# Kernel optimization log

Measured on AMD Instinct MI355X. Metric: run time of the kernel, lower is better.

The kernel has to match this reference:

```python
import jax, jax.numpy as jnp
import numpy as np

L = 2
S = (L + 1) ** 2            # 9 spherical harmonic coefficients
C = 128                     # sphere_channels
H = 128                     # hidden_channels
NH = 8                      # num_heads
A = 32                      # attn_alpha_channels
V = 16                      # attn_value_channels
N = 5000                    # nodes
E = 50000                   # edges
DE = 128                    # invariant edge embedding dim
G = 18                      # S2 grid points

# l of each coefficient in l-major layout [S]
L_OF = np.concatenate([np.full(2 * l + 1, l) for l in range(L + 1)])
IDX_M0 = np.array([l * l + l for l in range(L + 1)])

def _idx_m(m):
    neg = np.array([l * l + l - m for l in range(m, L + 1)])
    pos = np.array([l * l + l + m for l in range(m, L + 1)])
    return neg, pos

IDX_M1_NEG, IDX_M1_POS = _idx_m(1)
IDX_M2_NEG, IDX_M2_POS = _idx_m(2)
# m-major ordering and its inverse permutation back to l-major
PERM = np.concatenate([IDX_M0, IDX_M1_POS, IDX_M1_NEG, IDX_M2_POS, IDX_M2_NEG])
INV_PERM = np.argsort(PERM)


def _silu(x):
    return x * jax.nn.sigmoid(x)


def _layernorm(x, g, b, eps=1e-5):
    mu = x.mean(-1, keepdims=True)
    var = ((x - mu) ** 2).mean(-1, keepdims=True)
    return (x - mu) * jax.lax.rsqrt(var + eps) * g + b


def _smooth_leaky_relu(x, a=0.2):
    return 0.5 * (1 + a) * x + 0.5 * (1 - a) * x * (2 * jax.nn.sigmoid(x) - 1)


def _so2_conv(x, w_m0, b_m0, w_m1, w_m2, cout):
    """SO(2) convolution on rotated embeddings. x: [E,S,Cin] l-major.
    Returns ([E,S,cout] l-major, extra m=0 channels)."""
    e = x.shape[0]
    # m = 0: plain linear over flattened (L+1)*Cin
    x0 = x[:, IDX_M0, :].reshape(e, -1)
    y0 = x0 @ w_m0 + b_m0
    y0_main = y0[:, : (L + 1) * cout].reshape(e, L + 1, cout)
    y0_extra = y0[:, (L + 1) * cout:]
    parts = [y0_main]
    # m > 0: complex (cos/sin) SO2 mixing with shared weight for real/imag
    for neg, pos, w in ((IDX_M1_NEG, IDX_M1_POS, w_m1), (IDX_M2_NEG, IDX_M2_POS, w_m2)):
        nl = len(neg)
        xr = x[:, pos, :].reshape(e, -1)
        xi = x[:, neg, :].reshape(e, -1)
        yr = xr @ w  # [E, 2*nl*cout]
        yi = xi @ w
        yr_r, yr_i = yr[:, : nl * cout], yr[:, nl * cout:]
        yi_r, yi_i = yi[:, : nl * cout], yi[:, nl * cout:]
        parts.append((yr_r - yi_i).reshape(e, nl, cout))   # +m (real)
        parts.append((yr_i + yi_r).reshape(e, nl, cout))   # -m (imag)
    out_m = jnp.concatenate(parts, axis=1)                 # m-major
    return out_m[:, INV_PERM, :], y0_extra


def _s2_act(x, togrid, fromgrid):
    g = jnp.einsum('gs,esc->egc', togrid, x)
    return jnp.einsum('sg,egc->esc', fromgrid, _silu(g))


def _sep_s2_act(scalars, x, togrid, fromgrid):
    t = _s2_act(x, togrid, fromgrid)
    return jnp.concatenate([_silu(scalars)[:, None, :], t[:, 1:, :]], axis=1)


def _so3_linear(x, w, b):
    # w: [L+1, Cin, Cout], shared across m within each l; bias only on l=0
    out = jnp.einsum('nsc,sco->nso', x, w[L_OF])
    return out.at[:, 0, :].add(b)


def _eqv_norm(x, g, b, eps=1e-5):
    # l=0: layernorm over channels; l>0: RMS over (m, channels) per degree
    outs = [_layernorm(x[:, 0:1, :], g[0], b)]
    for l in range(1, L + 1):
        sl = x[:, l * l:(l + 1) * (l + 1), :]
        rms = jnp.sqrt(jnp.mean(sl ** 2, axis=(1, 2), keepdims=True) + eps)
        outs.append(sl / rms * g[l])
    return jnp.concatenate(outs, axis=1)


def _forward(x, edge_distance, wigner, rad_w1, rad_b1, rad_ln_g, rad_ln_b, rad_w2, rad_b2,
             w1_m0, b1_m0, w1_m1, w1_m2, w2_m0, b2_m0, w2_m1, w2_m2,
             alpha_ln_g, alpha_ln_b, alpha_dot, proj_w, proj_b,
             norm1_g, norm1_b, norm2_g, norm2_b,
             gate_w, gate_b, ffn_w1, ffn_b1, ffn_w2, ffn_b2,
             togrid, fromgrid, edge_src, edge_dst):
    # ---------- SO2 equivariant graph attention ----------
    xn = _eqv_norm(x, norm1_g, norm1_b)
    msg = jnp.concatenate([xn[edge_src], xn[edge_dst]], axis=-1)      # [E,S,2C]
    msg = jnp.einsum('eij,ejc->eic', wigner, msg)                     # rotate to edge frame
    # radial function shared across m within each l (use_m_share_rad)
    h = _silu(_layernorm(edge_distance @ rad_w1 + rad_b1, rad_ln_g, rad_ln_b))
    rad = (h @ rad_w2 + rad_b2).reshape(-1, L + 1, 2 * C)             # [E,L+1,2C]
    msg = msg * rad[:, L_OF, :]
    hid, x0_extra = _so2_conv(msg, w1_m0, b1_m0, w1_m1, w1_m2, H)
    x_alpha = x0_extra[:, : NH * A].reshape(-1, NH, A)
    gating = x0_extra[:, NH * A:]                                     # [E,H]
    hid = _sep_s2_act(gating, hid, togrid, fromgrid)
    val, _ = _so2_conv(hid, w2_m0, b2_m0, w2_m1, w2_m2, NH * V)
    val = jnp.einsum('eji,ejc->eic', wigner, val)                     # rotate back (D^T)
    # attention weights with per-destination segment softmax
    a = _smooth_leaky_relu(_layernorm(x_alpha, alpha_ln_g, alpha_ln_b))
    a = jnp.einsum('eha,ha->eh', a, alpha_dot)                        # [E,NH]
    amax = jax.ops.segment_max(a, edge_dst, num_segments=N)
    aexp = jnp.exp(a - amax[edge_dst])
    asum = jax.ops.segment_sum(aexp, edge_dst, num_segments=N)
    attn = aexp / asum[edge_dst]
    msg_out = (val.reshape(-1, S, NH, V) * attn[:, None, :, None]).reshape(-1, S, NH * V)
    node = jax.ops.segment_sum(msg_out, edge_dst, num_segments=N)     # [N,S,NH*V]
    x = x + _so3_linear(node, proj_w, proj_b)
    # ---------- spherical FFN (sep S2 gating) ----------
    xn = _eqv_norm(x, norm2_g, norm2_b)
    gating = xn[:, 0, :] @ gate_w + gate_b
    hh = _so3_linear(xn, ffn_w1, ffn_b1)
    hh = _sep_s2_act(gating, hh, togrid, fromgrid)
    return x + _so3_linear(hh, ffn_w2, ffn_b2)


def setup_inputs() -> dict:
    key = jax.random.key(0)
    ks = iter(jax.random.split(key, 64))
    def nrm(shape, scale=1.0):
        return jax.random.normal(next(ks), shape, dtype=jnp.float32) * scale
    EX = NH * A + H
    inp = {}
    inp['x'] = nrm((N, S, C))
    inp['edge_distance'] = nrm((E, DE))
    inp['wigner'] = nrm((E, S, S), 1.0 / np.sqrt(S))
    inp['rad_w1'] = nrm((DE, 64), 1.0 / np.sqrt(DE)); inp['rad_b1'] = jnp.zeros((64,), jnp.float32)
    inp['rad_ln_g'] = jnp.ones((64,), jnp.float32); inp['rad_ln_b'] = jnp.zeros((64,), jnp.float32)
    inp['rad_w2'] = nrm((64, 2 * C * (L + 1)), 0.05); inp['rad_b2'] = jnp.ones((2 * C * (L + 1),), jnp.float32)
    inp['w1_m0'] = nrm(((L + 1) * 2 * C, (L + 1) * H + EX), 1.0 / np.sqrt((L + 1) * 2 * C))
    inp['b1_m0'] = jnp.zeros(((L + 1) * H + EX,), jnp.float32)
    inp['w1_m1'] = nrm((2 * 2 * C, 2 * 2 * H), 1.0 / np.sqrt(2 * 2 * C))
    inp['w1_m2'] = nrm((2 * C, 2 * H), 1.0 / np.sqrt(2 * C))
    inp['w2_m0'] = nrm(((L + 1) * H, (L + 1) * NH * V), 1.0 / np.sqrt((L + 1) * H))
    inp['b2_m0'] = jnp.zeros(((L + 1) * NH * V,), jnp.float32)
    inp['w2_m1'] = nrm((2 * H, 2 * 2 * NH * V), 1.0 / np.sqrt(2 * H))
    inp['w2_m2'] = nrm((H, 2 * NH * V), 1.0 / np.sqrt(H))
    inp['alpha_ln_g'] = jnp.ones((A,), jnp.float32); inp['alpha_ln_b'] = jnp.zeros((A,), jnp.float32)
    inp['alpha_dot'] = nrm((NH, A), 1.0 / np.sqrt(A))
    inp['proj_w'] = nrm((L + 1, NH * V, C), 1.0 / np.sqrt(NH * V)); inp['proj_b'] = jnp.zeros((C,), jnp.float32)
    inp['norm1_g'] = jnp.ones((L + 1, C), jnp.float32); inp['norm1_b'] = jnp.zeros((C,), jnp.float32)
    inp['norm2_g'] = jnp.ones((L + 1, C), jnp.float32); inp['norm2_b'] = jnp.zeros((C,), jnp.float32)
    inp['gate_w'] = nrm((C, H), 1.0 / np.sqrt(C)); inp['gate_b'] = jnp.zeros((H,), jnp.float32)
    inp['ffn_w1'] = nrm((L + 1, C, H), 1.0 / np.sqrt(C)); inp['ffn_b1'] = jnp.zeros((H,), jnp.float32)
    inp['ffn_w2'] = nrm((L + 1, H, C), 1.0 / np.sqrt(H)); inp['ffn_b2'] = jnp.zeros((C,), jnp.float32)
    inp['togrid'] = nrm((G, S), 1.0 / np.sqrt(S))
    inp['fromgrid'] = nrm((S, G), 1.0 / np.sqrt(G))
    inp['edge_src'] = jax.random.randint(next(ks), (E,), 0, N)
    inp['edge_dst'] = jax.random.randint(next(ks), (E,), 0, N)
    return inp


def reference(x, edge_distance, wigner, rad_w1, rad_b1, rad_ln_g, rad_ln_b, rad_w2, rad_b2,
              w1_m0, b1_m0, w1_m1, w1_m2, w2_m0, b2_m0, w2_m1, w2_m2,
              alpha_ln_g, alpha_ln_b, alpha_dot, proj_w, proj_b,
              norm1_g, norm1_b, norm2_g, norm2_b,
              gate_w, gate_b, ffn_w1, ffn_b1, ffn_w2, ffn_b2,
              togrid, fromgrid, edge_src, edge_dst):
    return _forward(x, edge_distance, wigner, rad_w1, rad_b1, rad_ln_g, rad_ln_b, rad_w2, rad_b2,
                    w1_m0, b1_m0, w1_m1, w1_m2, w2_m0, b2_m0, w2_m1, w2_m2,
                    alpha_ln_g, alpha_ln_b, alpha_dot, proj_w, proj_b,
                    norm1_g, norm1_b, norm2_g, norm2_b,
                    gate_w, gate_b, ffn_w1, ffn_b1, ffn_w2, ffn_b2,
                    togrid, fromgrid, edge_src, edge_dst)
```

## Files before the change

kernel.cpp:

```cpp
#include <hip/hip_runtime.h>
#include <hip/hip_bf16.h>

typedef unsigned short u16;
typedef unsigned int   u32;
typedef __attribute__((ext_vector_type(8))) short short8;
typedef __attribute__((ext_vector_type(4))) float float4v;

#define NN 5000
#define EE 50000

__device__ __forceinline__ float b2f(u16 u){ return __uint_as_float(((u32)u)<<16); }
__device__ __forceinline__ u16 f2b(float f){
  u32 x = __float_as_uint(f);
  u32 r = (x + 0x7fffu + ((x>>16)&1u)) >> 16;
  return (u16)r;
}
__device__ __forceinline__ float ldin(const void* p, size_t i, bool f32){
  return f32 ? ((const float*)p)[i] : b2f(((const u16*)p)[i]);
}
__device__ __forceinline__ float siluf(float x){ return x/(1.f+__expf(-x)); }
__device__ __forceinline__ float waveRedSum(float v){
  #pragma unroll
  for (int m=32;m>=1;m>>=1) v += __shfl_xor(v,m,64);
  return v;
}
__device__ __forceinline__ float red32(float v){
  #pragma unroll
  for (int m=16;m>=1;m>>=1) v += __shfl_xor(v,m,64);
  return v;
}
__device__ __forceinline__ void gload_lds16(const u16* g, u16* l){
  __builtin_amdgcn_global_load_lds((const __attribute__((address_space(1))) void*)g,
                                   (__attribute__((address_space(3))) void*)l, 16, 0, 0);
}


__global__ __launch_bounds__(256) void zero_kernel(float* __restrict__ p, int n){
  for (int i = blockIdx.x*256 + threadIdx.x; i < n; i += gridDim.x*256) p[i] = 0.f;
}

__global__ void detect_kernel(const u32* __restrict__ ng, int* __restrict__ flag){
  if (blockIdx.x == 0 && threadIdx.x == 0) *flag = (ng[0] == 0x3F800000u) ? 1 : 0;
}

__global__ __launch_bounds__(256) void hist_kernel(const int* __restrict__ edst,
    int* __restrict__ counts){
  int e = blockIdx.x*256 + threadIdx.x;
  if (e < EE) atomicAdd(&counts[edst[e]], 1);
}

__global__ __launch_bounds__(1024) void scan_kernel(const int* __restrict__ counts,
    int* __restrict__ row_start, int* __restrict__ cursor){
  __shared__ int buf[1024];
  __shared__ int base;
  const int t = threadIdx.x;
  if (t == 0){ base = 0; row_start[0] = 0; }
  __syncthreads();
  for (int i0 = 0; i0 < NN; i0 += 1024){
    int i = i0 + t;
    int c = (i < NN) ? counts[i] : 0;
    buf[t] = c;
    __syncthreads();
    #pragma unroll
    for (int ofs = 1; ofs < 1024; ofs <<= 1){
      int v = (t >= ofs) ? buf[t-ofs] : 0;
      __syncthreads();
      buf[t] += v;
      __syncthreads();
    }
    if (i < NN){
      int incl = base + buf[t];
      row_start[i+1] = incl;
      cursor[i] = incl - c;
    }
    __syncthreads();
    if (t == 0) base += buf[1023];
    __syncthreads();
  }
}

__global__ __launch_bounds__(256) void place_kernel(const int* __restrict__ edst,
    int* __restrict__ cursor, int* __restrict__ order){
  int e = blockIdx.x*256 + threadIdx.x;
  if (e < EE) order[atomicAdd(&cursor[edst[e]], 1)] = e;
}

__global__ __launch_bounds__(256) void gathercvt_kernel(const int* __restrict__ dflag,
    const void* __restrict__ src, const int* __restrict__ order, int e0,
    u16* __restrict__ dst, int n){
  const bool f32 = (*dflag != 0);
  for (int i = blockIdx.x*256 + threadIdx.x; i < n; i += gridDim.x*256){
    int le = i >> 7, c = i & 127;
    int eg = order[e0 + le];
    dst[i] = f2b(ldin(src, (size_t)eg*128 + c, f32));
  }
}

__device__ __forceinline__ void do_cvtT(bool f32, const void* src, u16* dst,
    int K, int N, int tid, int stride){
  int total = K*N;
  for (int i = tid; i < total; i += stride){
    int n = i / K, k = i - n*K;
    dst[i] = f2b(ldin(src, (size_t)k*N + n, f32));
  }
}
__device__ __forceinline__ void do_cvtT3(bool f32, const void* src, u16* dst,
    int tid, int stride){
  for (int i = tid; i < 49152; i += stride){
    int l = i >> 14, j = i & 16383;
    int n = j >> 7, k = j & 127;
    dst[i] = f2b(ldin(src, (size_t)l*16384 + (size_t)k*128 + n, f32));
  }
}
__device__ __forceinline__ void do_wprepT(bool f32, const void* w, u16* wt,
    int K0, int N0, int tid, int stride){
  int total = 4*N0*K0;
  for (int i = tid; i < total; i += stride){
    int c = i / (2*K0), rr0 = i - c*2*K0;
    float v;
    if (rr0 < K0) v = ldin(w, (size_t)rr0*2*N0 + c, f32);
    else {
      int rr = rr0 - K0;
      if (c < N0) v = -ldin(w, (size_t)rr*2*N0 + N0 + c, f32);
      else        v =  ldin(w, (size_t)rr*2*N0 + (c - N0), f32);
    }
    wt[i] = f2b(v);
  }
}

__global__ __launch_bounds__(256) void prep_all_kernel(const int* __restrict__ dflag,
    const void* w1_m0, const void* w2_m0, const void* rad_w1, const void* rad_w2,
    const void* proj_w, const void* ffn_w1, const void* ffn_w2, const void* gate_w,
    const void* b1, const void* b2, const void* rb1, const void* rb2,
    const void* pb, const void* gb, const void* f1, const void* f2,
    const void* w1_m1, const void* w1_m2, const void* w2_m1, const void* w2_m2,
    u16* w1m0T, u16* w2m0T, u16* rw1T, u16* rw2T,
    u16* projT3, u16* ffn1T3, u16* ffn2T3, u16* gateT,
    u16* b1m0C, u16* b2m0C, u16* rb1C, u16* rb2C,
    u16* pbC, u16* gbC, u16* fb1C, u16* fb2C,
    u16* W1cT, u16* W2cT, u16* W3cT, u16* W4cT){
  const bool f32 = (*dflag != 0);
  const int tid = blockIdx.x*256 + threadIdx.x;
  const int stride = gridDim.x*256;
  switch (blockIdx.y){
    case 0:  do_cvtT (f32, w1_m0, w1m0T, 768, 768, tid, stride); break;
    case 1:  do_cvtT (f32, w2_m0, w2m0T, 384, 384, tid, stride); break;
    case 2:  do_cvtT (f32, rad_w1, rw1T, 128, 64,  tid, stride); break;
    case 3:  do_cvtT (f32, rad_w2, rw2T, 64, 768,  tid, stride); break;
    case 4:  do_cvtT3(f32, proj_w, projT3, tid, stride); break;
    case 5:  do_cvtT3(f32, ffn_w1, ffn1T3, tid, stride); break;
    case 6:  do_cvtT3(f32, ffn_w2, ffn2T3, tid, stride); break;
    case 7:  do_cvtT (f32, gate_w, gateT, 128, 128, tid, stride); break;
    case 8:
      if (tid < 768) b1m0C[tid] = f2b(ldin(b1, tid, f32));
      if (tid < 384) b2m0C[tid] = f2b(ldin(b2, tid, f32));
      if (tid < 64)  rb1C[tid]  = f2b(ldin(rb1, tid, f32));
      if (tid < 768) rb2C[tid]  = f2b(ldin(rb2, tid, f32));
      if (tid < 128){
        pbC[tid]  = f2b(ldin(pb, tid, f32));
        gbC[tid]  = f2b(ldin(gb, tid, f32));
        fb1C[tid] = f2b(ldin(f1, tid, f32));
        fb2C[tid] = f2b(ldin(f2, tid, f32));
      }
      break;
    case 9:  do_wprepT(f32, w1_m1, W1cT, 512, 256, tid, stride); break;
    case 10: do_wprepT(f32, w1_m2, W2cT, 256, 128, tid, stride); break;
    case 11: do_wprepT(f32, w2_m1, W3cT, 256, 256, tid, stride); break;
    case 12: do_wprepT(f32, w2_m2, W4cT, 128, 128, tid, stride); break;
  }
}

__global__ __launch_bounds__(128) void eqvnorm_kernel(const int* __restrict__ dflag,
    const void* __restrict__ x, int in_always_f32,
    const void* __restrict__ g, const void* __restrict__ b,
    void* __restrict__ out, int out_f32){
  const bool f32 = (*dflag != 0);
  const bool inf32 = in_always_f32 || f32;
  const int n = blockIdx.x, t = threadIdx.x;
  __shared__ float red[2];
  float v[9];
  #pragma unroll
  for (int s=0;s<9;s++) v[s] = ldin(x, (size_t)n*1152 + s*128 + t, inf32);

  auto bsum = [&](float val)->float{
    float w = waveRedSum(val);
    __syncthreads();
    if ((t & 63) == 0) red[t>>6] = w;
    __syncthreads();
    return red[0] + red[1];
  };
  auto store = [&](int idx, float val){
    if (out_f32) ((float*)out)[(size_t)n*1152 + idx] = val;
    else         ((u16*) out)[(size_t)n*1152 + idx] = f2b(val);
  };
  float mu  = bsum(v[0]) * (1.f/128.f);
  float d0  = v[0] - mu;
  float var = bsum(d0*d0) * (1.f/128.f);
  store(t, d0 * rsqrtf(var + 1e-5f) * ldin(g, t, f32) + ldin(b, t, f32));
  float ss1 = v[1]*v[1] + v[2]*v[2] + v[3]*v[3];
  float inv1 = rsqrtf(bsum(ss1)*(1.f/384.f) + 1e-5f);
  float g1 = ldin(g, 128 + t, f32);
  #pragma unroll
  for (int s=1;s<=3;s++) store(s*128 + t, v[s]*inv1*g1);
  float ss2 = 0.f;
  #pragma unroll
  for (int s=4;s<9;s++) ss2 += v[s]*v[s];
  float inv2 = rsqrtf(bsum(ss2)*(1.f/640.f) + 1e-5f);
  float g2 = ldin(g, 256 + t, f32);
  #pragma unroll
  for (int s=4;s<9;s++) store(s*128 + t, v[s]*inv2*g2);
}

__global__ __launch_bounds__(256) void gemm_mfma_kernel(
    const u16* __restrict__ A, int lda, int K,
    const u16* __restrict__ Wt, int NOUT,
    const u16* __restrict__ bias,
    u16* __restrict__ out0, int ld0, int coloff0, int split,
    u16* __restrict__ out1, int ld1, int M){
  __shared__ __align__(16) u16 As[2][128*32];
  __shared__ __align__(16) u16 Bs[2][128*32];
  const int t = threadIdx.x;
  const int nxg = gridDim.x, nyg = gridDim.y;
  const int nwg = nxg * nyg;
  const int bid = blockIdx.y * nxg + blockIdx.x;
  const int q = nwg >> 3, r = nwg & 7;
  const int xcd = bid & 7, sid = bid >> 3;
  const int swz = (xcd < r ? xcd*(q+1) : r*(q+1) + (xcd - r)*q) + sid;
  const int mt = swz / nyg;
  const int r0 = mt * 128;
  const int n0 = (swz - mt*nyg) * 128;
  const int lane = t & 63, wave = t >> 6;
  const int wr = (wave & 1) * 64, wn = (wave >> 1) * 64;
  float4v acc[4][4];
  #pragma unroll
  for (int i=0;i<4;i++)
    #pragma unroll
    for (int j=0;j<4;j++) acc[i][j] = (float4v){0.f,0.f,0.f,0.f};

  const int fr = lane & 15, fq = (lane >> 4) * 8;

  const int Rw   = wave * 32;
  const int srow = lane >> 2;
  const int scol = (lane & 3) * 8;
  const u16* aG0 = A  + (size_t)(r0 + Rw + srow) * lda + scol;
  const u16* aG1 = aG0 + (size_t)16 * lda;
  const bool aV0 = (r0 + Rw + srow)      < M;
  const bool aV1 = (r0 + Rw + 16 + srow) < M;
  const u16* bG0 = Wt + (size_t)(n0 + Rw + srow) * K + scol;
  const u16* bG1 = bG0 + (size_t)16 * K;
  const bool bV0 = (n0 + Rw + srow)      < NOUT;
  const bool bV1 = (n0 + Rw + 16 + srow) < NOUT;

  auto stage = [&](int buf, int k0){
    u16* lA = &As[buf][Rw * 32];
    u16* lB = &Bs[buf][Rw * 32];
    if (aV0) gload_lds16(aG0 + k0, lA);
    if (aV1) gload_lds16(aG1 + k0, lA + 16*32);
    if (bV0) gload_lds16(bG0 + k0, lB);
    if (bV1) gload_lds16(bG1 + k0, lB + 16*32);
  };

  stage(0, 0);
  __syncthreads();
  int cur = 0;
  for (int k0 = 0; k0 < K; k0 += 32){
    const int k1 = k0 + 32;
    if (k1 < K) stage(cur ^ 1, k1);
    short8 af[4], bfv[4];
    #pragma unroll
    for (int i=0;i<4;i++){
      af[i]  = *(const short8*)&As[cur][(wr + i*16 + fr)*32 + fq];
      bfv[i] = *(const short8*)&Bs[cur][(wn + i*16 + fr)*32 + fq];
    }
    #pragma unroll
    for (int i=0;i<4;i++)
      #pragma unroll
      for (int j=0;j<4;j++)
        acc[i][j] = __builtin_amdgcn_mfma_f32_16x16x32_bf16(af[i], bfv[j], acc[i][j], 0, 0, 0);
    __syncthreads();
    cur ^= 1;
  }
  const int quad = lane >> 4;
  #pragma unroll
  for (int j=0;j<4;j++){
    int col = n0 + wn + j*16 + fr;
    if (col >= NOUT) continue;
    float bv = bias ? b2f(bias[col]) : 0.f;
    #pragma unroll
    for (int i=0;i<4;i++){
      int rbase = r0 + wr + i*16 + quad*4;
      #pragma unroll
      for (int rg=0; rg<4; rg++){
        int row = rbase + rg;
        if (row >= M) continue;
        float v = acc[i][j][rg] + bv;
        if (col < split) out0[(size_t)row*ld0 + coloff0 + col] = f2b(v);
        else             out1[(size_t)row*ld1 + (col - split)] = f2b(v);
      }
    }
  }
}

__global__ __launch_bounds__(256) void gemm_node_kernel(
    const int* __restrict__ dflag,
    const u16* __restrict__ A,
    const u16* __restrict__ W3t,
    const u16* __restrict__ bias,
    const void* __restrict__ resid, int resid_mode,
    void* __restrict__ out, int out_mode, int gate_out){
  const bool f32 = (*dflag != 0);
  const int l = blockIdx.y;
  const int rpn  = (l==0) ? 1 : ((l==1) ? 3 : 5);
  const int soff = (l==0) ? 0 : ((l==1) ? 1 : 4);
  const int M = NN * rpn;
  const int r0 = blockIdx.x * 128;
  if (r0 >= M) return;
  __shared__ __align__(16) u16 As[128][40];
  __shared__ __align__(16) u16 Bs[128][40];
  const int t = threadIdx.x;
  const int lane = t & 63, wave = t >> 6;
  const int wr = (wave & 1) * 64, wn = (wave >> 1) * 64;
  float4v acc[4][4];
  #pragma unroll
  for (int i=0;i<4;i++)
    #pragma unroll
    for (int j=0;j<4;j++) acc[i][j] = (float4v){0.f,0.f,0.f,0.f};

  const int sr = t >> 2, sc = (t & 3) * 8;
  const int fr = lane & 15, fq = (lane >> 4) * 8;
  size_t abase[2]; bool aval[2];
  #pragma unroll
  for (int s2=0;s2<2;s2++){
    int m = r0 + sr + s2*64;
    aval[s2] = m < M;
    int n = m / rpn, srow = soff + (m % rpn);
    abase[s2] = (size_t)n*1152 + srow*128 + sc;
  }
  const u16* Wl = W3t + (size_t)l*16384;

  #pragma unroll
  for (int k0 = 0; k0 < 128; k0 += 32){
    #pragma unroll
    for (int s2=0;s2<2;s2++){
      int row = sr + s2*64;
      uint4 av = make_uint4(0u,0u,0u,0u);
      if (aval[s2]) av = *(const uint4*)(A + abase[s2] + k0);
      *(uint4*)&As[row][sc] = av;
      uint4 wv = *(const uint4*)(Wl + (size_t)row*128 + k0 + sc);
      *(uint4*)&Bs[row][sc] = wv;
    }
    __syncthreads();
    short8 af[4], bfr[4];
    #pragma unroll
    for (int i=0;i<4;i++){
      af[i]  = *(const short8*)&As[wr + i*16 + fr][fq];
      bfr[i] = *(const short8*)&Bs[wn + i*16 + fr][fq];
    }
    #pragma unroll
    for (int i=0;i<4;i++)
      #pragma unroll
      for (int j=0;j<4;j++)
        acc[i][j] = __builtin_amdgcn_mfma_f32_16x16x32_bf16(af[i], bfr[j], acc[i][j], 0, 0, 0);
    __syncthreads();
  }
  const int quad = lane >> 4;
  #pragma unroll
  for (int j=0;j<4;j++){
    int col = wn + j*16 + fr;
    float bv = (bias && l==0) ? b2f(bias[col]) : 0.f;
    #pragma unroll
    for (int i=0;i<4;i++){
      int rbase = r0 + wr + i*16 + quad*4;
      #pragma unroll
      for (int rg=0; rg<4; rg++){
        int m = rbase + rg;
        if (m >= M) continue;
        int n = m / rpn, srow = soff + (m % rpn);
        size_t na = (size_t)n*1152 + srow*128 + col;
        float v = acc[i][j][rg] + bv;
        if (resid_mode == 1)      v += ((const float*)resid)[na];
        else if (resid_mode == 2) v += ldin(resid, na, f32);
        if (gate_out)            ((u16*)out)[(size_t)n*128 + col] = f2b(v);
        else if (out_mode == 0)  ((u16*)out)[na] = f2b(v);
        else if (out_mode == 1)  ((float*)out)[na] = v;
        else { if (f32) ((float*)out)[na] = v; else ((u16*)out)[na] = f2b(v); }
      }
    }
  }
}

__global__ __launch_bounds__(256) void nodecvt_kernel(const float* __restrict__ node,
    const float* __restrict__ nsum, u16* __restrict__ nodeb){
  for (int i = blockIdx.x*256 + threadIdx.x; i < NN*1152; i += gridDim.x*256){
    int n = i / 1152, c = i & 127, h = c >> 4;
    float ns = nsum[(size_t)n*8 + h];
    float rs = (ns > 0.f) ? 1.f/ns : 0.f;
    nodeb[i] = f2b(node[i] * rs);
  }
}

__global__ __launch_bounds__(128) void node_s2act_kernel(const int* __restrict__ dflag,
    const u16* __restrict__ hh, const u16* __restrict__ gating,
    const void* __restrict__ tg, const void* __restrict__ fg, u16* __restrict__ hh2){
  const bool f32 = (*dflag != 0);
  const int n = blockIdx.x, t = threadIdx.x;
  __shared__ float TG[162], FG[162];
  for (int i=t; i<162; i+=128){ TG[i]=ldin(tg,i,f32); FG[i]=ldin(fg,i,f32); }
  float hv[9];
  #pragma unroll
  for (int s=0;s<9;s++) hv[s] = b2f(hh[(size_t)n*1152 + s*128 + t]);
  __syncthreads();
  float gg[18];
  #pragma unroll
  for (int gi=0;gi<18;gi++){
    float a = 0.f;
    #pragma unroll
    for (int s=0;s<9;s++) a = fmaf(TG[gi*9+s], hv[s], a);
    gg[gi] = siluf(a);
  }
  hh2[(size_t)n*1152 + t] = f2b(siluf(b2f(gating[(size_t)n*128 + t])));
  #pragma unroll
  for (int s=1;s<9;s++){
    float a = 0.f;
    #pragma unroll
    for (int gi=0;gi<18;gi++) a = fmaf(FG[s*18+gi], gg[gi], a);
    hh2[(size_t)n*1152 + s*128 + t] = f2b(a);
  }
}

__global__ __launch_bounds__(256) void lnsilu_kernel(const int* __restrict__ dflag,
    u16* __restrict__ H, const void* __restrict__ rlng, const void* __restrict__ rlnb, int M){
  const bool f32 = (*dflag != 0);
  const int r = blockIdx.x*4 + (threadIdx.x >> 6), lane = threadIdx.x & 63;
  if (r >= M) return;
  float h = b2f(H[(size_t)r*64 + lane]);
  float mu = waveRedSum(h) * (1.f/64.f);
  float d = h - mu;
  float var = waveRedSum(d*d) * (1.f/64.f);
  float hn = d * rsqrtf(var + 1e-5f) * ldin(rlng, lane, f32) + ldin(rlnb, lane, f32);
  H[(size_t)r*64 + lane] = f2b(siluf(hn));
}

__global__ __launch_bounds__(256) void edge_rot_kernel(const int* __restrict__ dflag,
    const u16* __restrict__ xn, const void* __restrict__ wig,
    const u16* __restrict__ rad,
    const int* __restrict__ esrc, const int* __restrict__ edst,
    const int* __restrict__ order, int e0, u16* __restrict__ msg){
  const bool f32 = (*dflag != 0);
  const int le = blockIdx.x, t = threadIdx.x;
  const int eg = order[e0 + le];
  __shared__ float W[81];
  if (t < 81) W[t] = ldin(wig, (size_t)eg*81 + t, f32);
  const int src = esrc[eg], dst = edst[eg];
  float pre[9];
  const u16* base = (t < 128) ? (xn + (size_t)src*1152 + t) : (xn + (size_t)dst*1152 + (t-128));
  #pragma unroll
  for (int j=0;j<9;j++) pre[j] = b2f(base[j*128]);
  __syncthreads();
  float rot[9];
  #pragma unroll
  for (int i=0;i<9;i++){
    float a = 0.f;
    #pragma unroll
    for (int j=0;j<9;j++) a = fmaf(W[i*9+j], pre[j], a);
    rot[i] = a;
  }
  float r[3];
  #pragma unroll
  for (int l=0;l<3;l++) r[l] = b2f(rad[(size_t)le*768 + l*256 + t]);
  const int INVP[9] = {0,5,1,3,8,6,2,4,7};
  const int LOF[9]  = {0,1,1,1,2,2,2,2,2};
  u16* mb = msg + (size_t)le*2304 + t;
  #pragma unroll
  for (int i=0;i<9;i++) mb[INVP[i]*256] = f2b(rot[i] * r[LOF[i]]);
}

__global__ __launch_bounds__(256) void s2act_alpha_kernel(const int* __restrict__ dflag,
    const u16* __restrict__ hid, const u16* __restrict__ extra,
    const void* __restrict__ togrid, const void* __restrict__ fromgrid,
    const void* __restrict__ alng, const void* __restrict__ alnb, const void* __restrict__ adot,
    const int* __restrict__ edst, const int* __restrict__ order, int e0,
    u16* __restrict__ hid2, float* __restrict__ aexp, float* __restrict__ nsum){
  const bool f32 = (*dflag != 0);
  const int le = blockIdx.x, t = threadIdx.x;
  const int p = e0 + le;
  __shared__ float TG[162], FG[162];
  if (t < 162){ TG[t] = ldin(togrid, t, f32); FG[t] = ldin(fromgrid, t, f32); }
  {
    const int h = t >> 5, ai = t & 31;
    float v = b2f(extra[(size_t)le*384 + t]);
    float mu = red32(v) * (1.f/32.f);
    float d = v - mu;
    float var = red32(d*d) * (1.f/32.f);
    float xh = d * rsqrtf(var + 1e-5f) * ldin(alng, ai, f32) + ldin(alnb, ai, f32);
    float sig = 1.f/(1.f + __expf(-xh));
    float sl = 0.6f*xh + 0.4f*xh*(2.f*sig - 1.f);
    float pp = sl * ldin(adot, h*32 + ai, f32);
    float dot = red32(pp);
    if (ai == 0){
      float ex = __expf(dot - 8.f);
      aexp[(size_t)p*8 + h] = ex;
      atomicAdd(&nsum[(size_t)edst[order[p]]*8 + h], ex);
    }
  }
  __syncthreads();
  if (t < 128){
    const int INVP[9] = {0,5,1,3,8,6,2,4,7};
    float hv[9];
    #pragma unroll
    for (int s=0;s<9;s++) hv[s] = b2f(hid[(size_t)le*1152 + INVP[s]*128 + t]);
    float gg[18];
    #pragma unroll
    for (int gi=0;gi<18;gi++){
      float a = 0.f;
      #pragma unroll
      for (int s=0;s<9;s++) a = fmaf(TG[gi*9+s], hv[s], a);
      gg[gi] = siluf(a);
    }
    hid2[(size_t)le*1152 + t] = f2b(siluf(b2f(extra[(size_t)le*384 + 256 + t])));
    #pragma unroll
    for (int s=1;s<9;s++){
      float a = 0.f;
      #pragma unroll
      for (int gi=0;gi<18;gi++) a = fmaf(FG[s*18+gi], gg[gi], a);
      hid2[(size_t)le*1152 + INVP[s]*128 + t] = f2b(a);
    }
  }
}

__global__ __launch_bounds__(128) void unrot_gather_kernel(const int* __restrict__ dflag,
    const u16* __restrict__ val, const void* __restrict__ wig,
    const float* __restrict__ aexp, const int* __restrict__ order,
    const int* __restrict__ row_start, int e0, int Mc, float* __restrict__ node){
  const bool f32 = (*dflag != 0);
  const int n = blockIdx.x, t = threadIdx.x;
  const int s = row_start[n], tend = row_start[n+1];
  int lo = (s > e0) ? s : e0;
  int hi = (tend < e0 + Mc) ? tend : (e0 + Mc);
  if (lo >= hi) return;
  __shared__ float W[81];
  __shared__ float SC[8];
  const int INVP[9] = {0,5,1,3,8,6,2,4,7};
  float acc[9];
  #pragma unroll
  for (int i=0;i<9;i++) acc[i] = 0.f;
  for (int p = lo; p < hi; p++){
    const int le = p - e0;
    const int eg = order[p];
    __syncthreads();
    if (t < 81) W[t] = ldin(wig, (size_t)eg*81 + t, f32);
    if (t >= 120) SC[t-120] = aexp[(size_t)p*8 + (t-120)];
    __syncthreads();
    float vs[9];
    #pragma unroll
    for (int j=0;j<9;j++) vs[j] = b2f(val[(size_t)le*1152 + INVP[j]*128 + t]);
    const float sc = SC[t>>4];
    #pragma unroll
    for (int i=0;i<9;i++){
      float a = 0.f;
      #pragma unroll
      for (int j=0;j<9;j++) a = fmaf(W[j*9+i], vs[j], a);
      acc[i] = fmaf(a, sc, acc[i]);
    }
  }
  const bool full = (s >= e0) && (tend <= e0 + Mc);
  #pragma unroll
  for (int i=0;i<9;i++){
    float* dst = &node[(size_t)n*1152 + i*128 + t];
    if (full) *dst = acc[i];
    else      atomicAdd(dst, acc[i]);
  }
}

extern "C" void kernel_launch(void* const* d_in, const int* in_sizes, int n_in,
                              void* d_out, int out_size, void* d_ws, size_t ws_size,
                              hipStream_t stream){
  (void)in_sizes; (void)n_in; (void)out_size;
  const void* x       = d_in[0];
  const void* edist   = d_in[1];
  const void* wig     = d_in[2];
  const void* rad_w1  = d_in[3];
  const void* rad_b1  = d_in[4];
  const void* rad_lng = d_in[5];
  const void* rad_lnb = d_in[6];
  const void* rad_w2  = d_in[7];
  const void* rad_b2  = d_in[8];
  const void* w1_m0   = d_in[9];
  const void* b1_m0   = d_in[10];
  const void* w1_m1   = d_in[11];
  const void* w1_m2   = d_in[12];
  const void* w2_m0   = d_in[13];
  const void* b2_m0   = d_in[14];
  const void* w2_m1   = d_in[15];
  const void* w2_m2   = d_in[16];
  const void* alng    = d_in[17];
  const void* alnb    = d_in[18];
  const void* adot    = d_in[19];
  const void* proj_w  = d_in[20];
  const void* proj_b  = d_in[21];
  const void* norm1_g = d_in[22];
  const void* norm1_b = d_in[23];
  const void* norm2_g = d_in[24];
  const void* norm2_b = d_in[25];
  const void* gate_w  = d_in[26];
  const void* gate_b  = d_in[27];
  const void* ffn_w1  = d_in[28];
  const void* ffn_b1  = d_in[29];
  const void* ffn_w2  = d_in[30];
  const void* ffn_b2  = d_in[31];
  const void* togrid  = d_in[32];
  const void* fromgrid= d_in[33];
  const int* esrc     = (const int*)d_in[34];
  const int* edst     = (const int*)d_in[35];

  char* wsp = (char*)d_ws;
  size_t off = 0;
  auto alloc = [&](size_t bytes)->char*{
    char* p = wsp + off;
    off = (off + bytes + 255) & ~(size_t)255;
    return p;
  };
  int*  dflag  = (int*) alloc(4);
  u16*  W1cT   = (u16*) alloc((size_t)512*1024*2);
  u16*  W2cT   = (u16*) alloc((size_t)256*512*2);
  u16*  W3cT   = (u16*) alloc((size_t)512*512*2);
  u16*  W4cT   = (u16*) alloc((size_t)256*256*2);
  u16*  w1m0T  = (u16*) alloc((size_t)768*768*2);
  u16*  b1m0C  = (u16*) alloc((size_t)768*2);
  u16*  w2m0T  = (u16*) alloc((size_t)384*384*2);
  u16*  b2m0C  = (u16*) alloc((size_t)384*2);
  u16*  rw1T   = (u16*) alloc((size_t)64*128*2);
  u16*  rb1C   = (u16*) alloc((size_t)64*2);
  u16*  rw2T   = (u16*) alloc((size_t)768*64*2);
  u16*  rb2C   = (u16*) alloc((size_t)768*2);
  u16*  projT3 = (u16*) alloc((size_t)3*16384*2);
  u16*  ffn1T3 = (u16*) alloc((size_t)3*16384*2);
  u16*  ffn2T3 = (u16*) alloc((size_t)3*16384*2);
  u16*  gateT  = (u16*) alloc((size_t)16384*2);
  u16*  pbC    = (u16*) alloc((size_t)128*2);
  u16*  gbC    = (u16*) alloc((size_t)128*2);
  u16*  fb1C   = (u16*) alloc((size_t)128*2);
  u16*  fb2C   = (u16*) alloc((size_t)128*2);
  u16*  xn     = (u16*) alloc((size_t)NN*1152*2);
  float* aexp  = (float*)alloc((size_t)EE*8*4);
  float* nsum  = (float*)alloc((size_t)NN*8*4);
  float* node  = (float*)alloc((size_t)NN*1152*4);
  int*  counts = (int*) alloc((size_t)NN*4);
  int*  row_st = (int*) alloc((size_t)(NN+1)*4);
  int*  cursor = (int*) alloc((size_t)NN*4);
  int*  order  = (int*) alloc((size_t)EE*4);
  size_t fixed_end = off;
  size_t avail = (ws_size > fixed_end) ? (ws_size - fixed_end) : 0;

  long long cap = ((long long)avail - 4096) / 7680;
  int Ec;
  if (cap >= 50048) Ec = 50048;
  else {
    long long c128 = cap & ~127LL;
    if (c128 < 128) c128 = 128;
    int nch = (EE + (int)c128 - 1) / (int)c128;
    Ec = ((EE + nch - 1) / nch + 127) & ~127;
  }
  char* cb = wsp + fixed_end;
  u16* msgC   = (u16*)cb;
  u16* hidC   = (u16*)(cb + (size_t)Ec*2304*2);
  u16* extraC = (u16*)(cb + (size_t)Ec*2304*2 + (size_t)Ec*1152*2);
  u16* hid2C  = msgC;
  u16* valC   = hidC;
  u16* edistC = msgC;
  u16* radC   = hidC;
  u16* HrawC  = hidC + (size_t)Ec*768;
  u16*  nodeb  = (u16*)cb;
  float* xnew  = (float*)(cb + (size_t)NN*1152*2);
  u16*  xn2    = (u16*)(cb + (size_t)NN*1152*2 + (size_t)NN*1152*4);
  u16*  gating = xn2 + (size_t)NN*1152;
  u16*  hh     = gating + (size_t)NN*128;
  u16*  hh2    = hh + (size_t)NN*1152;

  detect_kernel<<<1, 64, 0, stream>>>((const u32*)norm1_g, dflag);

  zero_kernel<<<2048, 256, 0, stream>>>(nsum, NN*8 + NN*1152 + NN);

  hist_kernel<<<(EE+255)/256, 256, 0, stream>>>(edst, counts);
  scan_kernel<<<1, 1024, 0, stream>>>(counts, row_st, cursor);
  place_kernel<<<(EE+255)/256, 256, 0, stream>>>(edst, cursor, order);

  prep_all_kernel<<<dim3(256,13), 256, 0, stream>>>(dflag,
      w1_m0, w2_m0, rad_w1, rad_w2, proj_w, ffn_w1, ffn_w2, gate_w,
      b1_m0, b2_m0, rad_b1, rad_b2, proj_b, gate_b, ffn_b1, ffn_b2,
      w1_m1, w1_m2, w2_m1, w2_m2,
      w1m0T, w2m0T, rw1T, rw2T, projT3, ffn1T3, ffn2T3, gateT,
      b1m0C, b2m0C, rb1C, rb2C, pbC, gbC, fb1C, fb2C,
      W1cT, W2cT, W3cT, W4cT);

  eqvnorm_kernel<<<NN, 128, 0, stream>>>(dflag, x, 0, norm1_g, norm1_b, xn, 0);

  for (int e0 = 0; e0 < EE; e0 += Ec){
    int Mc = (EE - e0 < Ec) ? (EE - e0) : Ec;
    int GX = (Mc + 127) / 128;
    gathercvt_kernel<<<dim3((Mc*128+255)/256), 256, 0, stream>>>(dflag, edist, order, e0,
                                                                 edistC, Mc*128);
    gemm_mfma_kernel<<<dim3(GX,1), 256, 0, stream>>>(edistC, 128, 128, rw1T, 64, rb1C,
                                                     HrawC, 64, 0, 64, nullptr, 0, Mc);
    lnsilu_kernel<<<dim3((Mc+3)/4), 256, 0, stream>>>(dflag, HrawC, rad_lng, rad_lnb, Mc);
    gemm_mfma_kernel<<<dim3(GX,6), 256, 0, stream>>>(HrawC, 64, 64, rw2T, 768, rb2C,
                                                     radC, 768, 0, 768, nullptr, 0, Mc);
    edge_rot_kernel<<<Mc, 256, 0, stream>>>(dflag, xn, wig, radC, esrc, edst, order, e0, msgC);
    gemm_mfma_kernel<<<dim3(GX,6), 256, 0, stream>>>(msgC,        2304, 768,  w1m0T, 768, b1m0C,
                                                     hidC, 1152, 0,   384, extraC, 384, Mc);
    gemm_mfma_kernel<<<dim3(GX,4), 256, 0, stream>>>(msgC + 768,  2304, 1024, W1cT,  512, nullptr,
                                                     hidC, 1152, 384, 512, nullptr, 0, Mc);
    gemm_mfma_kernel<<<dim3(GX,2), 256, 0, stream>>>(msgC + 1792, 2304, 512,  W2cT,  256, nullptr,
                                                     hidC, 1152, 896, 256, nullptr, 0, Mc);
    s2act_alpha_kernel<<<Mc, 256, 0, stream>>>(dflag, hidC, extraC, togrid, fromgrid, alng,
                                               alnb, adot, edst, order, e0, hid2C, aexp, nsum);
    gemm_mfma_kernel<<<dim3(GX,3), 256, 0, stream>>>(hid2C,       1152, 384, w2m0T, 384, b2m0C,
                                                     valC, 1152, 0,   384, nullptr, 0, Mc);
    gemm_mfma_kernel<<<dim3(GX,4), 256, 0, stream>>>(hid2C + 384, 1152, 512, W3cT,  512, nullptr,
                                                     valC, 1152, 384, 512, nullptr, 0, Mc);
    gemm_mfma_kernel<<<dim3(GX,2), 256, 0, stream>>>(hid2C + 896, 1152, 256, W4cT,  256, nullptr,
                                                     valC, 1152, 896, 256, nullptr, 0, Mc);
    unrot_gather_kernel<<<NN, 128, 0, stream>>>(dflag, valC, wig, aexp, order, row_st,
                                                e0, Mc, node);
  }

  const int GN2 = (NN*5 + 127)/128;
  nodecvt_kernel<<<2048, 256, 0, stream>>>(node, nsum, nodeb);
  gemm_node_kernel<<<dim3(GN2,3), 256, 0, stream>>>(dflag, nodeb, projT3, pbC,
                                                    x, 2, xnew, 1, 0);
  eqvnorm_kernel<<<NN, 128, 0, stream>>>(dflag, xnew, 1, norm2_g, norm2_b, xn2, 0);
  gemm_node_kernel<<<dim3((NN+127)/128,1), 256, 0, stream>>>(dflag, xn2, gateT, gbC,
                                                             nullptr, 0, gating, 0, 1);
  gemm_node_kernel<<<dim3(GN2,3), 256, 0, stream>>>(dflag, xn2, ffn1T3, fb1C,
                                                    nullptr, 0, hh, 0, 0);
  node_s2act_kernel<<<NN, 128, 0, stream>>>(dflag, hh, gating, togrid, fromgrid, hh2);
  gemm_node_kernel<<<dim3(GN2,3), 256, 0, stream>>>(dflag, hh2, ffn2T3, fb2C,
                                                    xnew, 1, d_out, 2, 0);
}
```

Baseline: 1.174 ms.

## Batch the three SO(2) conv GEMMs into one launch and preconvert S2 grid matrices

Each triple of per-m GEMM launches (m=0, m=1, m=2) inside the edge-chunk loop becomes a single gemm_mfma3_kernel launch. It dispatches tiles to one of three job descriptors by grid-y index, which cuts launch count and fills the GPU better with one combined grid. The togrid/fromgrid matrices are converted once to fp32 in the prep kernel. The S2 activation kernels then read them directly from global memory instead of staging them into shared memory behind a __syncthreads, and their loops are reordered so each hv value is used across all grid points. The risk is the per-block job-selection branch and uneven tile cost across jobs with different K.

After: 1.043 ms. 11.1% less time.

```diff
diff --git a/kernel.cpp b/kernel.cpp
--- a/kernel.cpp
+++ b/kernel.cpp
@@ -134,11 +134,13 @@
     const void* b1, const void* b2, const void* rb1, const void* rb2,
     const void* pb, const void* gb, const void* f1, const void* f2,
     const void* w1_m1, const void* w1_m2, const void* w2_m1, const void* w2_m2,
+    const void* togrid, const void* fromgrid,
     u16* w1m0T, u16* w2m0T, u16* rw1T, u16* rw2T,
     u16* projT3, u16* ffn1T3, u16* ffn2T3, u16* gateT,
     u16* b1m0C, u16* b2m0C, u16* rb1C, u16* rb2C,
     u16* pbC, u16* gbC, u16* fb1C, u16* fb2C,
-    u16* W1cT, u16* W2cT, u16* W3cT, u16* W4cT){
+    u16* W1cT, u16* W2cT, u16* W3cT, u16* W4cT,
+    float* TGf, float* FGf){
   const bool f32 = (*dflag != 0);
   const int tid = blockIdx.x*256 + threadIdx.x;
   const int stride = gridDim.x*256;
@@ -167,6 +169,10 @@
     case 10: do_wprepT(f32, w1_m2, W2cT, 256, 128, tid, stride); break;
     case 11: do_wprepT(f32, w2_m1, W3cT, 256, 256, tid, stride); break;
     case 12: do_wprepT(f32, w2_m2, W4cT, 128, 128, tid, stride); break;
+    case 13:
+      if (tid < 162) TGf[tid] = ldin(togrid, tid, f32);
+      else if (tid >= 256 && tid < 418) FGf[tid-256] = ldin(fromgrid, tid-256, f32);
+      break;
   }
 }
 
@@ -211,24 +217,13 @@
   for (int s=4;s<9;s++) store(s*128 + t, v[s]*inv2*g2);
 }
 
-__global__ __launch_bounds__(256) void gemm_mfma_kernel(
+__device__ __forceinline__ void gemm_core(u16* AsB, u16* BsB,
     const u16* __restrict__ A, int lda, int K,
     const u16* __restrict__ Wt, int NOUT,
     const u16* __restrict__ bias,
     u16* __restrict__ out0, int ld0, int coloff0, int split,
-    u16* __restrict__ out1, int ld1, int M){
-  __shared__ __align__(16) u16 As[2][128*32];
-  __shared__ __align__(16) u16 Bs[2][128*32];
+    u16* __restrict__ out1, int ld1, int M, int r0, int n0){
   const int t = threadIdx.x;
-  const int nxg = gridDim.x, nyg = gridDim.y;
-  const int nwg = nxg * nyg;
-  const int bid = blockIdx.y * nxg + blockIdx.x;
-  const int q = nwg >> 3, r = nwg & 7;
-  const int xcd = bid & 7, sid = bid >> 3;
-  const int swz = (xcd < r ? xcd*(q+1) : r*(q+1) + (xcd - r)*q) + sid;
-  const int mt = swz / nyg;
-  const int r0 = mt * 128;
-  const int n0 = (swz - mt*nyg) * 128;
   const int lane = t & 63, wave = t >> 6;
   const int wr = (wave & 1) * 64, wn = (wave >> 1) * 64;
   float4v acc[4][4];
@@ -252,8 +247,8 @@
   const bool bV1 = (n0 + Rw + 16 + srow) < NOUT;
 
   auto stage = [&](int buf, int k0){
-    u16* lA = &As[buf][Rw * 32];
-    u16* lB = &Bs[buf][Rw * 32];
+    u16* lA = AsB + buf*4096 + Rw * 32;
+    u16* lB = BsB + buf*4096 + Rw * 32;
     if (aV0) gload_lds16(aG0 + k0, lA);
     if (aV1) gload_lds16(aG1 + k0, lA + 16*32);
     if (bV0) gload_lds16(bG0 + k0, lB);
@@ -269,8 +264,8 @@
     short8 af[4], bfv[4];
     #pragma unroll
     for (int i=0;i<4;i++){
-      af[i]  = *(const short8*)&As[cur][(wr + i*16 + fr)*32 + fq];
-      bfv[i] = *(const short8*)&Bs[cur][(wn + i*16 + fr)*32 + fq];
+      af[i]  = *(const short8*)&AsB[cur*4096 + (wr + i*16 + fr)*32 + fq];
+      bfv[i] = *(const short8*)&BsB[cur*4096 + (wn + i*16 + fr)*32 + fq];
     }
     #pragma unroll
     for (int i=0;i<4;i++)
@@ -299,6 +294,49 @@
       }
     }
   }
+}
+
+__device__ __forceinline__ int xcd_swz(int bid, int nwg){
+  const int q = nwg >> 3, r = nwg & 7;
+  const int xcd = bid & 7, sid = bid >> 3;
+  return (xcd < r ? xcd*(q+1) : r*(q+1) + (xcd - r)*q) + sid;
+}
+
+__global__ __launch_bounds__(256) void gemm_mfma_kernel(
+    const u16* __restrict__ A, int lda, int K,
+    const u16* __restrict__ Wt, int NOUT,
+    const u16* __restrict__ bias,
+    u16* __restrict__ out0, int ld0, int coloff0, int split,
+    u16* __restrict__ out1, int ld1, int M){
+  __shared__ __align__(16) u16 As[2][128*32];
+  __shared__ __align__(16) u16 Bs[2][128*32];
+  const int nxg = gridDim.x, nyg = gridDim.y;
+  const int bid = blockIdx.y * nxg + blockIdx.x;
+  const int swz = xcd_swz(bid, nxg*nyg);
+  const int mt = swz / nyg;
+  gemm_core(&As[0][0], &Bs[0][0], A, lda, K, Wt, NOUT, bias,
+            out0, ld0, coloff0, split, out1, ld1, M, mt*128, (swz - mt*nyg)*128);
+}
+
+struct GemmJob {
+  const u16* A; const u16* Wt; const u16* bias; u16* out0; u16* out1;
+  int lda, K, NOUT, ld0, coloff0, split, ld1;
+};
+__global__ __launch_bounds__(256) void gemm_mfma3_kernel(
+    GemmJob j0, GemmJob j1, GemmJob j2, int ny0, int ny01, int M){
+  __shared__ __align__(16) u16 As[2][128*32];
+  __shared__ __align__(16) u16 Bs[2][128*32];
+  const int nxg = gridDim.x, nyg = gridDim.y;
+  const int bid = blockIdx.y * nxg + blockIdx.x;
+  const int swz = xcd_swz(bid, nxg*nyg);
+  const int mt = swz / nyg;
+  const int y  = swz - mt*nyg;
+  GemmJob j; int yt;
+  if (y < ny0)       { j = j0; yt = y; }
+  else if (y < ny01) { j = j1; yt = y - ny0; }
+  else               { j = j2; yt = y - ny01; }
+  gemm_core(&As[0][0], &Bs[0][0], j.A, j.lda, j.K, j.Wt, j.NOUT, j.bias,
+            j.out0, j.ld0, j.coloff0, j.split, j.out1, j.ld1, M, mt*128, yt*128);
 }
 
 __global__ __launch_bounds__(256) void gemm_node_kernel(
@@ -399,31 +437,30 @@
   }
 }
 
-__global__ __launch_bounds__(128) void node_s2act_kernel(const int* __restrict__ dflag,
+__global__ __launch_bounds__(128) void node_s2act_kernel(
     const u16* __restrict__ hh, const u16* __restrict__ gating,
-    const void* __restrict__ tg, const void* __restrict__ fg, u16* __restrict__ hh2){
-  const bool f32 = (*dflag != 0);
+    const float* __restrict__ TGf, const float* __restrict__ FGf, u16* __restrict__ hh2){
   const int n = blockIdx.x, t = threadIdx.x;
-  __shared__ float TG[162], FG[162];
-  for (int i=t; i<162; i+=128){ TG[i]=ldin(tg,i,f32); FG[i]=ldin(fg,i,f32); }
   float hv[9];
   #pragma unroll
   for (int s=0;s<9;s++) hv[s] = b2f(hh[(size_t)n*1152 + s*128 + t]);
-  __syncthreads();
   float gg[18];
   #pragma unroll
-  for (int gi=0;gi<18;gi++){
-    float a = 0.f;
-    #pragma unroll
-    for (int s=0;s<9;s++) a = fmaf(TG[gi*9+s], hv[s], a);
-    gg[gi] = siluf(a);
-  }
+  for (int gi=0;gi<18;gi++) gg[gi] = 0.f;
+  #pragma unroll
+  for (int s=0;s<9;s++){
+    float hvs = hv[s];
+    #pragma unroll
+    for (int gi=0;gi<18;gi++) gg[gi] = fmaf(TGf[gi*9+s], hvs, gg[gi]);
+  }
+  #pragma unroll
+  for (int gi=0;gi<18;gi++) gg[gi] = siluf(gg[gi]);
   hh2[(size_t)n*1152 + t] = f2b(siluf(b2f(gating[(size_t)n*128 + t])));
   #pragma unroll
   for (int s=1;s<9;s++){
     float a = 0.f;
     #pragma unroll
-    for (int gi=0;gi<18;gi++) a = fmaf(FG[s*18+gi], gg[gi], a);
+    for (int gi=0;gi<18;gi++) a = fmaf(FGf[s*18+gi], gg[gi], a);
     hh2[(size_t)n*1152 + s*128 + t] = f2b(a);
   }
 }
@@ -477,15 +514,13 @@
 
 __global__ __launch_bounds__(256) void s2act_alpha_kernel(const int* __restrict__ dflag,
     const u16* __restrict__ hid, const u16* __restrict__ extra,
-    const void* __restrict__ togrid, const void* __restrict__ fromgrid,
+    const float* __restrict__ TGf, const float* __restrict__ FGf,
     const void* __restrict__ alng, const void* __restrict__ alnb, const void* __restrict__ adot,
     const int* __restrict__ edst, const int* __restrict__ order, int e0,
     u16* __restrict__ hid2, float* __restrict__ aexp, float* __restrict__ nsum){
   const bool f32 = (*dflag != 0);
   const int le = blockIdx.x, t = threadIdx.x;
   const int p = e0 + le;
-  __shared__ float TG[162], FG[162];
-  if (t < 162){ TG[t] = ldin(togrid, t, f32); FG[t] = ldin(fromgrid, t, f32); }
   {
     const int h = t >> 5, ai = t & 31;
     float v = b2f(extra[(size_t)le*384 + t]);
@@ -503,7 +538,6 @@
       atomicAdd(&nsum[(size_t)edst[order[p]]*8 + h], ex);
     }
   }
-  __syncthreads();
   if (t < 128){
     const int INVP[9] = {0,5,1,3,8,6,2,4,7};
     float hv[9];
@@ -511,18 +545,21 @@
     for (int s=0;s<9;s++) hv[s] = b2f(hid[(size_t)le*1152 + INVP[s]*128 + t]);
     float gg[18];
     #pragma unroll
-    for (int gi=0;gi<18;gi++){
-      float a = 0.f;
+    for (int gi=0;gi<18;gi++) gg[gi] = 0.f;
+    #pragma unroll
+    for (int s=0;s<9;s++){
+      float hvs = hv[s];
       #pragma unroll
-      for (int s=0;s<9;s++) a = fmaf(TG[gi*9+s], hv[s], a);
-      gg[gi] = siluf(a);
-    }
+      for (int gi=0;gi<18;gi++) gg[gi] = fmaf(TGf[gi*9+s], hvs, gg[gi]);
+    }
+    #pragma unroll
+    for (int gi=0;gi<18;gi++) gg[gi] = siluf(gg[gi]);
     hid2[(size_t)le*1152 + t] = f2b(siluf(b2f(extra[(size_t)le*384 + 256 + t])));
     #pragma unroll
     for (int s=1;s<9;s++){
       float a = 0.f;
       #pragma unroll
-      for (int gi=0;gi<18;gi++) a = fmaf(FG[s*18+gi], gg[gi], a);
+      for (int gi=0;gi<18;gi++) a = fmaf(FGf[s*18+gi], gg[gi], a);
       hid2[(size_t)le*1152 + INVP[s]*128 + t] = f2b(a);
     }
   }
@@ -641,6 +678,8 @@
   u16*  gbC    = (u16*) alloc((size_t)128*2);
   u16*  fb1C   = (u16*) alloc((size_t)128*2);
   u16*  fb2C   = (u16*) alloc((size_t)128*2);
+  float* TGf   = (float*)alloc((size_t)162*4);
+  float* FGf   = (float*)alloc((size_t)162*4);
   u16*  xn     = (u16*) alloc((size_t)NN*1152*2);
   float* aexp  = (float*)alloc((size_t)EE*8*4);
   float* nsum  = (float*)alloc((size_t)NN*8*4);
@@ -685,13 +724,13 @@
   scan_kernel<<<1, 1024, 0, stream>>>(counts, row_st, cursor);
   place_kernel<<<(EE+255)/256, 256, 0, stream>>>(edst, cursor, order);
 
-  prep_all_kernel<<<dim3(256,13), 256, 0, stream>>>(dflag,
+  prep_all_kernel<<<dim3(256,14), 256, 0, stream>>>(dflag,
       w1_m0, w2_m0, rad_w1, rad_w2, proj_w, ffn_w1, ffn_w2, gate_w,
       b1_m0, b2_m0, rad_b1, rad_b2, proj_b, gate_b, ffn_b1, ffn_b2,
-      w1_m1, w1_m2, w2_m1, w2_m2,
+      w1_m1, w1_m2, w2_m1, w2_m2, togrid, fromgrid,
       w1m0T, w2m0T, rw1T, rw2T, projT3, ffn1T3, ffn2T3, gateT,
       b1m0C, b2m0C, rb1C, rb2C, pbC, gbC, fb1C, fb2C,
-      W1cT, W2cT, W3cT, W4cT);
+      W1cT, W2cT, W3cT, W4cT, TGf, FGf);
 
   eqvnorm_kernel<<<NN, 128, 0, stream>>>(dflag, x, 0, norm1_g, norm1_b, xn, 0);
 
@@ -706,20 +745,20 @@
     gemm_mfma_kernel<<<dim3(GX,6), 256, 0, stream>>>(HrawC, 64, 64, rw2T, 768, rb2C,
                                                      radC, 768, 0, 768, nullptr, 0, Mc);
     edge_rot_kernel<<<Mc, 256, 0, stream>>>(dflag, xn, wig, radC, esrc, edst, order, e0, msgC);
-    gemm_mfma_kernel<<<dim3(GX,6), 256, 0, stream>>>(msgC,        2304, 768,  w1m0T, 768, b1m0C,
-                                                     hidC, 1152, 0,   384, extraC, 384, Mc);
-    gemm_mfma_kernel<<<dim3(GX,4), 256, 0, stream>>>(msgC + 768,  2304, 1024, W1cT,  512, nullptr,
-                                                     hidC, 1152, 384, 512, nullptr, 0, Mc);
-    gemm_mfma_kernel<<<dim3(GX,2), 256, 0, stream>>>(msgC + 1792, 2304, 512,  W2cT,  256, nullptr,
-                                                     hidC, 1152, 896, 256, nullptr, 0, Mc);
-    s2act_alpha_kernel<<<Mc, 256, 0, stream>>>(dflag, hidC, extraC, togrid, fromgrid, alng,
+    {
+      GemmJob j0{msgC,        w1m0T, b1m0C,   hidC, extraC, 2304, 768,  768, 1152, 0,   384, 384};
+      GemmJob j1{msgC + 768,  W1cT,  nullptr, hidC, nullptr,2304, 1024, 512, 1152, 384, 512, 0};
+      GemmJob j2{msgC + 1792, W2cT,  nullptr, hidC, nullptr,2304, 512,  256, 1152, 896, 256, 0};
+      gemm_mfma3_kernel<<<dim3(GX,12), 256, 0, stream>>>(j0, j1, j2, 6, 10, Mc);
+    }
+    s2act_alpha_kernel<<<Mc, 256, 0, stream>>>(dflag, hidC, extraC, TGf, FGf, alng,
                                                alnb, adot, edst, order, e0, hid2C, aexp, nsum);
-    gemm_mfma_kernel<<<dim3(GX,3), 256, 0, stream>>>(hid2C,       1152, 384, w2m0T, 384, b2m0C,
-                                                     valC, 1152, 0,   384, nullptr, 0, Mc);
-    gemm_mfma_kernel<<<dim3(GX,4), 256, 0, stream>>>(hid2C + 384, 1152, 512, W3cT,  512, nullptr,
-                                                     valC, 1152, 384, 512, nullptr, 0, Mc);
-    gemm_mfma_kernel<<<dim3(GX,2), 256, 0, stream>>>(hid2C + 896, 1152, 256, W4cT,  256, nullptr,
-                                                     valC, 1152, 896, 256, nullptr, 0, Mc);
+    {
+      GemmJob j0{hid2C,       w2m0T, b2m0C,   valC, nullptr, 1152, 384, 384, 1152, 0,   384, 0};
+      GemmJob j1{hid2C + 384, W3cT,  nullptr, valC, nullptr, 1152, 512, 512, 1152, 384, 512, 0};
+      GemmJob j2{hid2C + 896, W4cT,  nullptr, valC, nullptr, 1152, 256, 256, 1152, 896, 256, 0};
+      gemm_mfma3_kernel<<<dim3(GX,9), 256, 0, stream>>>(j0, j1, j2, 3, 7, Mc);
+    }
     unrot_gather_kernel<<<NN, 128, 0, stream>>>(dflag, valC, wig, aexp, order, row_st,
                                                 e0, Mc, node);
   }
@@ -733,7 +772,7 @@
                                                              nullptr, 0, gating, 0, 1);
   gemm_node_kernel<<<dim3(GN2,3), 256, 0, stream>>>(dflag, xn2, ffn1T3, fb1C,
                                                     nullptr, 0, hh, 0, 0);
-  node_s2act_kernel<<<NN, 128, 0, stream>>>(dflag, hh, gating, togrid, fromgrid, hh2);
+  node_s2act_kernel<<<NN, 128, 0, stream>>>(hh, gating, TGf, FGf, hh2);
   gemm_node_kernel<<<dim3(GN2,3), 256, 0, stream>>>(dflag, hh2, ffn2T3, fb2C,
                                                     xnew, 1, d_out, 2, 0);
 }
```
